# Kernel optimization log

Measured on AMD Instinct MI355X. Metric: run time of the kernel, lower is better.

The kernel has to match this reference:

```python
import jax, jax.numpy as jnp
import numpy as np

N, E, G = 100000, 1600000, 256   # nodes, edges, graphs
D, H, OUT, STEPS = 128, 128, 2, 4
EPS = 1e-5


def _bn(x, g, b):
    # BatchNorm1d training-mode math: biased batch stats
    mu = jnp.mean(x, axis=0)
    var = jnp.var(x, axis=0)
    return g * (x - mu) * jax.lax.rsqrt(var + EPS) + b


def setup_inputs() -> dict:
    key = jax.random.key(0)
    ks = jax.random.split(key, 20)
    s = 0.05
    return {
        "x": jax.random.normal(ks[0], (N, D), dtype=jnp.float32),
        "edge_index": jax.random.randint(ks[1], (2, E), 0, N, dtype=jnp.int32),
        "batch": jnp.sort(jax.random.randint(ks[2], (N,), 0, G, dtype=jnp.int32)),
        "W_in": jax.random.normal(ks[3], (H, D), dtype=jnp.float32) * s,
        "b_in": jnp.zeros((H,), jnp.float32),
        "bn1_g": jnp.ones((H,), jnp.float32),
        "bn1_b": jnp.zeros((H,), jnp.float32),
        "ggc_w": jax.random.normal(ks[4], (STEPS, H, H), dtype=jnp.float32) * s,
        "gru_wih": jax.random.normal(ks[5], (3 * H, H), dtype=jnp.float32) * s,
        "gru_whh": jax.random.normal(ks[6], (3 * H, H), dtype=jnp.float32) * s,
        "gru_bih": jnp.zeros((3 * H,), jnp.float32),
        "gru_bhh": jnp.zeros((3 * H,), jnp.float32),
        "bn2_g": jnp.ones((H,), jnp.float32),
        "bn2_b": jnp.zeros((H,), jnp.float32),
        "W1": jax.random.normal(ks[7], (H, 2 * H), dtype=jnp.float32) * s,
        "b1": jnp.zeros((H,), jnp.float32),
        "bn3_g": jnp.ones((H,), jnp.float32),
        "bn3_b": jnp.zeros((H,), jnp.float32),
        "W2": jax.random.normal(ks[8], (OUT, H), dtype=jnp.float32) * s,
        "b2": jnp.zeros((OUT,), jnp.float32),
    }


def reference(x, edge_index, batch, W_in, b_in, bn1_g, bn1_b, ggc_w,
              gru_wih, gru_whh, gru_bih, gru_bhh, bn2_g, bn2_b,
              W1, b1, bn3_g, bn3_b, W2, b2):
    src, dst = edge_index[0], edge_index[1]

    h = x @ W_in.T + b_in
    h = jax.nn.relu(_bn(h, bn1_g, bn1_b))
    skip = h

    # GatedGraphConv: per-step linear -> scatter-add aggregation -> GRUCell
    for i in range(STEPS):
        m = h @ ggc_w[i]                                   # [N,H]
        agg = jax.ops.segment_sum(m[src], dst, num_segments=N)  # [N,H]
        gi = agg @ gru_wih.T + gru_bih                     # [N,3H]
        gh = h @ gru_whh.T + gru_bhh                       # [N,3H]
        i_r, i_z, i_n = jnp.split(gi, 3, axis=1)
        h_r, h_z, h_n = jnp.split(gh, 3, axis=1)
        r = jax.nn.sigmoid(i_r + h_r)
        z = jax.nn.sigmoid(i_z + h_z)
        n = jnp.tanh(i_n + r * h_n)
        h = (1.0 - z) * n + z * h

    h = jax.nn.relu(_bn(h, bn2_g, bn2_b) + skip)

    # global_mean_pool (source uses it for both "mean" and "max" branches)
    cnt = jnp.maximum(jax.ops.segment_sum(jnp.ones((N,), h.dtype), batch, num_segments=G), 1.0)
    mean = jax.ops.segment_sum(h, batch, num_segments=G) / cnt[:, None]  # [G,H]
    pooled = jnp.concatenate([mean, mean], axis=1)                        # [G,2H]

    y = jax.nn.relu(_bn(pooled @ W1.T + b1, bn3_g, bn3_b))
    return y @ W2.T + b2
```

## Files before the change

kernel.cpp:

```cpp
#include <hip/hip_runtime.h>
#include <math.h>


#define EPSV 1e-5f

typedef __attribute__((ext_vector_type(8))) short bf16x8;
typedef __attribute__((ext_vector_type(4))) float f32x4;

__device__ __forceinline__ float fsig(float x){
  return 1.0f/(1.0f+__expf(-x));
}
__device__ __forceinline__ float ftanh(float x){
  float ax = fabsf(x);
  float e = __expf(-2.0f*ax);
  float r = (1.0f-e)/(1.0f+e);
  return copysignf(r, x);
}
__device__ __forceinline__ unsigned short bf16rne(float x){
  unsigned u = __float_as_uint(x);
  unsigned r = (u + 0x7FFFu + ((u>>16)&1u)) >> 16;
  return (unsigned short)r;
}
__device__ __forceinline__ float bf16tof(unsigned short h){
  return __uint_as_float(((unsigned)h)<<16);
}

__global__ void k_zero(float* __restrict__ p, int n){
  int i = blockIdx.x*256+threadIdx.x;
  if (i<n) p[i]=0.0f;
}

__global__ void k_prep(const float* __restrict__ Win, float* __restrict__ Wq,
                       const float* __restrict__ W1, float* __restrict__ W1cT){
  int i = blockIdx.x*256+threadIdx.x;
  if (i < 16384){
    int k=i>>7, j=i&127;
    Wq[(k>>2)*512 + j*4 + (k&3)] = Win[j*128+k];
  } else if (i < 32768){
    int r=i-16384; int j=r>>7, o=r&127;
    W1cT[j*128+o] = W1[o*256+j] + W1[o*256+128+j];
  }
}

__global__ void k_prepB(const float* __restrict__ ggc, const float* __restrict__ wih,
                        const float* __restrict__ whh,
                        short* __restrict__ Bhi, short* __restrict__ Blo){
  int i = blockIdx.x*256+threadIdx.x;
  int st = i>>17;
  int r  = i&131071;
  int k  = r>>9;
  int c  = r&511;
  int gr = c>>7, j = c&127;
  float val = 0.f;
  if (k<128){
    if (gr<3){
      const float* g = ggc + st*16384 + k*128;
      const float* w = wih + (gr*128+j)*128;
      float acc=0.f;
      for (int m=0;m<128;m++) acc += g[m]*w[m];
      val = acc;
    }
  } else {
    int kh = k-128;
    if (gr!=2){
      int gate = (gr==3)?2:gr;
      val = whh[(gate*128+j)*128 + kh];
    }
  }
  unsigned short h = bf16rne(val);
  unsigned short lo = bf16rne(val - bf16tof(h));
  size_t off = (size_t)st*131072 + ((size_t)(k>>5)*512 + (size_t)c)*32 + (size_t)(k&31);
  Bhi[off]=(short)h; Blo[off]=(short)lo;
}

__global__ __launch_bounds__(256,2) void k_gemm_in(
    const float* __restrict__ x, const float* __restrict__ Wq, const float* __restrict__ bin,
    float* __restrict__ X, float* __restrict__ sumP, float* __restrict__ sqP, int N)
{
  __shared__ __align__(16) float xl[32][128];
  __shared__ float red[2][128];
  int t=threadIdx.x;
  int nbase = blockIdx.x*32;
  for (int it=0; it<4; ++it){
    int f4 = it*256+t;
    int n = f4>>5; int k=(f4&31)*4;
    int gn=nbase+n;
    float4 v = make_float4(0.f,0.f,0.f,0.f);
    if (gn<N) v = *(const float4*)&x[(size_t)gn*128+k];
    *(float4*)&xl[n][k]=v;
  }
  __syncthreads();
  int j=t&127, half=t>>7, nb=half*16;
  float acc[16];
  #pragma unroll
  for (int q=0;q<16;q++) acc[q]=0.f;
  for (int k=0;k<128;k+=4){
    float4 w = *(const float4*)&Wq[(k>>2)*512 + j*4];
    #pragma unroll
    for (int q=0;q<16;q++){
      float4 xv = *(const float4*)&xl[nb+q][k];
      acc[q] += xv.x*w.x + xv.y*w.y + xv.z*w.z + xv.w*w.w;
    }
  }
  float bv = bin[j];
  float ts=0.f, tq=0.f;
  #pragma unroll
  for (int q=0;q<16;q++){
    int n=nbase+nb+q;
    if (n<N){
      float tv=acc[q]+bv;
      X[(size_t)n*128+j]=tv;
      ts+=tv; tq+=tv*tv;
    }
  }
  int p = (blockIdx.x&63)*128+j;
  red[half][j]=ts; __syncthreads();
  if (half==0) atomicAdd(&sumP[p], red[0][j]+red[1][j]);
  __syncthreads();
  red[half][j]=tq; __syncthreads();
  if (half==0) atomicAdd(&sqP[p], red[0][j]+red[1][j]);
}

__global__ void k_bn_fin(const float* __restrict__ sumP, const float* __restrict__ sqP, int P, float invcnt,
                         const float* __restrict__ g, const float* __restrict__ b,
                         float* __restrict__ sc, float* __restrict__ sh){
  int j = threadIdx.x;
  if (j>=128) return;
  float s=0.f,q=0.f;
  for (int p=0;p<P;p++){ s+=sumP[p*128+j]; q+=sqP[p*128+j]; }
  float mu = s*invcnt;
  float var = fmaxf(q*invcnt - mu*mu, 0.f);
  float scale = g[j]*rsqrtf(var+EPSV);
  sc[j]=scale; sh[j]=b[j]-mu*scale;
}

__global__ void k_apply_bn1(const float4* __restrict__ X, const float* __restrict__ sc,
                            const float* __restrict__ sh, float4* __restrict__ h0, int total4){
  int i = blockIdx.x*256+threadIdx.x;
  if (i>=total4) return;
  float4 t = X[i];
  int j0 = (i*4)&127;
  float4 s = *(const float4*)&sc[j0];
  float4 b = *(const float4*)&sh[j0];
  float4 o;
  o.x = fmaxf(t.x*s.x+b.x, 0.f);
  o.y = fmaxf(t.y*s.y+b.y, 0.f);
  o.z = fmaxf(t.z*s.z+b.z, 0.f);
  o.w = fmaxf(t.w*s.w+b.w, 0.f);
  h0[i]=o;
}

__global__ void k_hist(const int* __restrict__ dst, int* __restrict__ deg, int E){
  int e = blockIdx.x*256+threadIdx.x;
  if (e<E) atomicAdd(&deg[dst[e]], 1);
}
__global__ void k_scan1(const int* __restrict__ deg, int* __restrict__ rowptr, int* __restrict__ bsum, int N){
  __shared__ int tmp[256];
  int t=threadIdx.x; int n=blockIdx.x*256+t;
  int v = (n<N)?deg[n]:0;
  tmp[t]=v;
  __syncthreads();
  for (int o=1;o<256;o<<=1){
    int add = (t>=o)? tmp[t-o] : 0;
    __syncthreads();
    tmp[t]+=add;
    __syncthreads();
  }
  if (n<N) rowptr[n+1]=tmp[t];
  if (t==255) bsum[blockIdx.x]=tmp[255];
}
__global__ void k_scan2(int* bsum, int nb, int* rowptr){
  __shared__ int tmp[512];
  int t=threadIdx.x;
  int v = (t<nb)? bsum[t] : 0;
  tmp[t]=v; __syncthreads();
  for (int o=1;o<512;o<<=1){
    int add = (t>=o)? tmp[t-o] : 0;
    __syncthreads();
    tmp[t]+=add;
    __syncthreads();
  }
  if (t<nb) bsum[t]=tmp[t]-v;
  if (t==0) rowptr[0]=0;
}
__global__ void k_scan3(int* rowptr, const int* __restrict__ bsum, int N){
  int n = blockIdx.x*256+threadIdx.x;
  if (n<N) rowptr[n+1] += bsum[blockIdx.x];
}
__global__ void k_fill(const int* __restrict__ ei, int* __restrict__ deg,
                       const int* __restrict__ rowptr, int* __restrict__ col, int E){
  int e = blockIdx.x*256+threadIdx.x;
  if (e<E){
    int d = ei[E+e];
    int old = atomicSub(&deg[d],1);
    col[rowptr[d] + old - 1] = ei[e];
  }
}

__global__ __launch_bounds__(256,8) void k_agg(
    const float* __restrict__ h, float* __restrict__ s,
    const int* __restrict__ rowptr, const int* __restrict__ col, int N)
{
  int wave = (blockIdx.x*256+threadIdx.x)>>6;
  int lane = threadIdx.x&63;
  if (wave>=N) return;
  int e = rowptr[wave], e1 = rowptr[wave+1];
  float2 a0=make_float2(0.f,0.f), a1=a0, a2=a0, a3=a0;
  for (; e+3<e1; e+=4){
    int c0=col[e],c1=col[e+1],c2=col[e+2],c3=col[e+3];
    float2 v0 = *(const float2*)&h[(size_t)c0*128+lane*2];
    float2 v1 = *(const float2*)&h[(size_t)c1*128+lane*2];
    float2 v2 = *(const float2*)&h[(size_t)c2*128+lane*2];
    float2 v3 = *(const float2*)&h[(size_t)c3*128+lane*2];
    a0.x+=v0.x; a0.y+=v0.y; a1.x+=v1.x; a1.y+=v1.y;
    a2.x+=v2.x; a2.y+=v2.y; a3.x+=v3.x; a3.y+=v3.y;
  }
  for (; e<e1; e++){
    int c0=col[e];
    float2 v0 = *(const float2*)&h[(size_t)c0*128+lane*2];
    a0.x+=v0.x; a0.y+=v0.y;
  }
  float2 r;
  r.x=(a0.x+a1.x)+(a2.x+a3.x);
  r.y=(a0.y+a1.y)+(a2.y+a3.y);
  *(float2*)&s[(size_t)wave*128+lane*2]=r;
}

__global__ __launch_bounds__(256,2) void k_gru_mfma(
    const float* __restrict__ s, const float* __restrict__ hin, float* __restrict__ hout,
    const short* __restrict__ Bhi, const short* __restrict__ Blo,
    const float* __restrict__ bih, const float* __restrict__ bhh, int N,
    float* __restrict__ sumP, float* __restrict__ sqP)
{
  __shared__ short Ahi[32*256];
  __shared__ short Alo[32*256];
  int t = threadIdx.x;
  int nbase = blockIdx.x*32;

  for (int it=0; it<8; ++it){
    int f4 = it*256 + t;
    int row = f4>>6;
    int c4  = f4&63;
    int k   = c4*4;
    int n   = nbase + row;
    float4 v = make_float4(0.f,0.f,0.f,0.f);
    if (n < N){
      const float* src = (k<128) ? &s[(size_t)n*128 + k] : &hin[(size_t)n*128 + (k-128)];
      v = *(const float4*)src;
    }
    unsigned short h0=bf16rne(v.x), h1=bf16rne(v.y), h2=bf16rne(v.z), h3=bf16rne(v.w);
    unsigned short l0=bf16rne(v.x-bf16tof(h0)), l1=bf16rne(v.y-bf16tof(h1));
    unsigned short l2=bf16rne(v.z-bf16tof(h2)), l3=bf16rne(v.w-bf16tof(h3));
    int g = c4>>1, half = c4&1;
    int gs = g ^ (row&7);
    int off = row*256 + gs*8 + half*4;
    uint2 H; H.x = (unsigned)h0 | ((unsigned)h1<<16); H.y = (unsigned)h2 | ((unsigned)h3<<16);
    uint2 L; L.x = (unsigned)l0 | ((unsigned)l1<<16); L.y = (unsigned)l2 | ((unsigned)l3<<16);
    *(uint2*)&Ahi[off] = H;
    *(uint2*)&Alo[off] = L;
  }
  __syncthreads();

  int wv = t>>6, l = t&63;
  int lj = l&15, lk = l>>4;

  f32x4 acc[2][8];
  #pragma unroll
  for (int mt=0; mt<2; ++mt)
    #pragma unroll
    for (int nt=0; nt<8; ++nt)
      acc[mt][nt] = (f32x4){0.f,0.f,0.f,0.f};

  for (int kc=0; kc<8; ++kc){
    bf16x8 a_hi[2], a_lo[2];
    #pragma unroll
    for (int mt=0; mt<2; ++mt){
      int r = mt*16 + lj;
      int g = kc*4 + lk;
      int off = r*256 + ((g ^ (r&7))<<3);
      a_hi[mt] = *(bf16x8*)&Ahi[off];
      a_lo[mt] = *(bf16x8*)&Alo[off];
    }
    #pragma unroll
    for (int gr=0; gr<4; ++gr){
      #pragma unroll
      for (int jt=0; jt<2; ++jt){
        int nt = gr*2 + jt;
        int c  = gr*128 + wv*32 + jt*16 + lj;
        size_t boff = ((size_t)kc*512 + (size_t)c)*32 + (size_t)lk*8;
        bf16x8 b_hi = *(const bf16x8*)&Bhi[boff];
        bf16x8 b_lo = *(const bf16x8*)&Blo[boff];
        acc[0][nt] = __builtin_amdgcn_mfma_f32_16x16x32_bf16(a_hi[0], b_hi, acc[0][nt], 0,0,0);
        acc[1][nt] = __builtin_amdgcn_mfma_f32_16x16x32_bf16(a_hi[1], b_hi, acc[1][nt], 0,0,0);
        acc[0][nt] = __builtin_amdgcn_mfma_f32_16x16x32_bf16(a_lo[0], b_hi, acc[0][nt], 0,0,0);
        acc[1][nt] = __builtin_amdgcn_mfma_f32_16x16x32_bf16(a_lo[1], b_hi, acc[1][nt], 0,0,0);
        acc[0][nt] = __builtin_amdgcn_mfma_f32_16x16x32_bf16(a_hi[0], b_lo, acc[0][nt], 0,0,0);
        acc[1][nt] = __builtin_amdgcn_mfma_f32_16x16x32_bf16(a_hi[1], b_lo, acc[1][nt], 0,0,0);
      }
    }
  }

  #pragma unroll
  for (int jt=0; jt<2; ++jt){
    int j = wv*32 + jt*16 + lj;
    float br=bih[j], bz=bih[128+j], bn_=bih[256+j];
    float cr=bhh[j], cz=bhh[128+j], cn=bhh[256+j];
    float ts=0.f, tq=0.f;
    #pragma unroll
    for (int mt=0; mt<2; ++mt){
      #pragma unroll
      for (int rg=0; rg<4; ++rg){
        int n = nbase + mt*16 + lk*4 + rg;
        if (n < N){
          float r  = fsig(acc[mt][0+jt][rg] + br + cr);
          float z  = fsig(acc[mt][2+jt][rg] + bz + cz);
          float nn = ftanh(acc[mt][4+jt][rg] + bn_ + r*(acc[mt][6+jt][rg] + cn));
          float hold = hin[(size_t)n*128 + j];
          float hv = (1.f-z)*nn + z*hold;
          hout[(size_t)n*128 + j] = hv;
          ts += hv; tq += hv*hv;
        }
      }
    }
    if (sumP){
      atomicAdd(&sumP[(blockIdx.x&63)*128 + j], ts);
      atomicAdd(&sqP [(blockIdx.x&63)*128 + j], tq);
    }
  }
}

__global__ void k_bn2_pool(const float* __restrict__ hfin, const float* __restrict__ h0,
                           const int* __restrict__ batch, const float* __restrict__ sc,
                           const float* __restrict__ sh, float* __restrict__ pool,
                           float* __restrict__ cntf, int N){
  int t=threadIdx.x, j=t&127, half=t>>7;
  int n0 = blockIdx.x*256 + half*128;
  float scv=sc[j], shv=sh[j];
  int curg=-1; float acc=0.f, cacc=0.f;
  for (int r=0;r<128;r++){
    int n=n0+r; if (n>=N) break;
    int g = batch[n];
    float v = fmaxf(hfin[(size_t)n*128+j]*scv+shv + h0[(size_t)n*128+j], 0.f);
    if (g!=curg){
      if (curg>=0){
        atomicAdd(&pool[curg*128+j], acc);
        if (j==0) atomicAdd(&cntf[curg], cacc);
      }
      curg=g; acc=0.f; cacc=0.f;
    }
    acc+=v; cacc+=1.f;
  }
  if (curg>=0){
    atomicAdd(&pool[curg*128+j], acc);
    if (j==0) atomicAdd(&cntf[curg], cacc);
  }
}

__global__ void k_head1(const float* __restrict__ pool, const float* __restrict__ cntf,
                        const float* __restrict__ W1cT, const float* __restrict__ b1,
                        float* __restrict__ t3, float* __restrict__ sum3, float* __restrict__ sq3){
  __shared__ float mean[128];
  int g=blockIdx.x, o=threadIdx.x;
  float inv = 1.0f/fmaxf(cntf[g],1.0f);
  mean[o] = pool[g*128+o]*inv;
  __syncthreads();
  float acc=0.f;
  for (int jj=0;jj<128;jj++) acc += mean[jj]*W1cT[jj*128+o];
  float v = acc + b1[o];
  t3[g*128+o]=v;
  atomicAdd(&sum3[o], v);
  atomicAdd(&sq3[o], v*v);
}

__global__ void k_head2(const float* __restrict__ t3, const float* __restrict__ sc,
                        const float* __restrict__ sh, const float* __restrict__ W2,
                        const float* __restrict__ b2, float* __restrict__ out){
  __shared__ float y[128];
  int g=blockIdx.x, o=threadIdx.x;
  float v = fmaxf(t3[g*128+o]*sc[o]+sh[o], 0.f);
  y[o]=v; __syncthreads();
  if (o<2){
    float acc=b2[o];
    for (int k=0;k<128;k++) acc += y[k]*W2[o*128+k];
    out[g*2+o]=acc;
  }
}

extern "C" void kernel_launch(void* const* d_in, const int* in_sizes, int n_in,
                              void* d_out, int out_size, void* d_ws, size_t ws_size,
                              hipStream_t stream){
  (void)n_in; (void)ws_size;
  const float* x    = (const float*)d_in[0];
  const int*   ei   = (const int*)d_in[1];
  const int*   batch= (const int*)d_in[2];
  const float* W_in = (const float*)d_in[3];
  const float* b_in = (const float*)d_in[4];
  const float* bn1_g= (const float*)d_in[5];
  const float* bn1_b= (const float*)d_in[6];
  const float* ggc  = (const float*)d_in[7];
  const float* wih  = (const float*)d_in[8];
  const float* whh  = (const float*)d_in[9];
  const float* bih  = (const float*)d_in[10];
  const float* bhh  = (const float*)d_in[11];
  const float* bn2_g= (const float*)d_in[12];
  const float* bn2_b= (const float*)d_in[13];
  const float* W1   = (const float*)d_in[14];
  const float* b1   = (const float*)d_in[15];
  const float* bn3_g= (const float*)d_in[16];
  const float* bn3_b= (const float*)d_in[17];
  const float* W2   = (const float*)d_in[18];
  const float* b2   = (const float*)d_in[19];
  float* out = (float*)d_out;

  int N = in_sizes[0]/128;
  int E = in_sizes[1]/2;
  int G = out_size/2;

  char* ws = (char*)d_ws;
  size_t off=0;
  auto alloc=[&](size_t bytes)->char*{
    char* p = ws+off; off = (off+bytes+255) & ~(size_t)255; return p;
  };
  float* buf0 = (float*)alloc((size_t)N*128*4);
  float* h0   = (float*)alloc((size_t)N*128*4);
  float* buf2 = (float*)alloc((size_t)N*128*4);
  short* Bhi  = (short*)alloc((size_t)4*131072*2);
  short* Blo  = (short*)alloc((size_t)4*131072*2);
  float* Wq   = (float*)alloc((size_t)16384*4);
  float* W1cT = (float*)alloc((size_t)16384*4);
  int* rowptr = (int*)alloc((size_t)(N+1)*4);
  int* col    = (int*)alloc((size_t)E*4);
  int* bsum   = (int*)alloc((size_t)512*4);
  float* t3   = (float*)alloc((size_t)G*128*4);
  float* sc1 = (float*)alloc(512); float* sh1 = (float*)alloc(512);
  float* sc2 = (float*)alloc(512); float* sh2 = (float*)alloc(512);
  float* sc3 = (float*)alloc(512); float* sh3 = (float*)alloc(512);
  char* zstart = ws+off;
  int*   deg  = (int*)alloc((size_t)N*4);
  float* sumP1= (float*)alloc((size_t)64*128*4);
  float* sqP1 = (float*)alloc((size_t)64*128*4);
  float* sumP2= (float*)alloc((size_t)64*128*4);
  float* sqP2 = (float*)alloc((size_t)64*128*4);
  float* sum3 = (float*)alloc(512);
  float* sq3  = (float*)alloc(512);
  float* pool = (float*)alloc((size_t)G*128*4);
  float* cntf = (float*)alloc((size_t)G*4);
  char* zend = ws+off;
  int zwords = (int)((zend - zstart)/4);

  int nbScan  = (N+255)/256;
  int gridN32 = (N+31)/32;
  int gridAgg = (N*64+255)/256;

  k_zero<<<(zwords+255)/256,256,0,stream>>>((float*)zstart, zwords);
  k_prep<<<128,256,0,stream>>>(W_in, Wq, W1, W1cT);
  k_prepB<<<2048,256,0,stream>>>(ggc, wih, whh, Bhi, Blo);

  k_hist<<<(E+255)/256,256,0,stream>>>(ei+E, deg, E);
  k_scan1<<<nbScan,256,0,stream>>>(deg, rowptr, bsum, N);
  k_scan2<<<1,512,0,stream>>>(bsum, nbScan, rowptr);
  k_scan3<<<nbScan,256,0,stream>>>(rowptr, bsum, N);
  k_fill<<<(E+255)/256,256,0,stream>>>(ei, deg, rowptr, col, E);

  k_gemm_in<<<gridN32,256,0,stream>>>(x, Wq, b_in, buf0, sumP1, sqP1, N);
  k_bn_fin<<<1,128,0,stream>>>(sumP1, sqP1, 64, 1.0f/(float)N, bn1_g, bn1_b, sc1, sh1);
  k_apply_bn1<<<(N*128/4+255)/256,256,0,stream>>>((const float4*)buf0, sc1, sh1, (float4*)h0, N*128/4);

  k_agg<<<gridAgg,256,0,stream>>>(h0,   buf0, rowptr, col, N);
  k_gru_mfma<<<gridN32,256,0,stream>>>(buf0, h0,   buf0, Bhi+0*131072, Blo+0*131072, bih, bhh, N, nullptr, nullptr);
  k_agg<<<gridAgg,256,0,stream>>>(buf0, buf2, rowptr, col, N);
  k_gru_mfma<<<gridN32,256,0,stream>>>(buf2, buf0, buf2, Bhi+1*131072, Blo+1*131072, bih, bhh, N, nullptr, nullptr);
  k_agg<<<gridAgg,256,0,stream>>>(buf2, buf0, rowptr, col, N);
  k_gru_mfma<<<gridN32,256,0,stream>>>(buf0, buf2, buf0, Bhi+2*131072, Blo+2*131072, bih, bhh, N, nullptr, nullptr);
  k_agg<<<gridAgg,256,0,stream>>>(buf0, buf2, rowptr, col, N);
  k_gru_mfma<<<gridN32,256,0,stream>>>(buf2, buf0, buf2, Bhi+3*131072, Blo+3*131072, bih, bhh, N, sumP2, sqP2);

  k_bn_fin<<<1,128,0,stream>>>(sumP2, sqP2, 64, 1.0f/(float)N, bn2_g, bn2_b, sc2, sh2);
  k_bn2_pool<<<(N+255)/256,256,0,stream>>>(buf2, h0, batch, sc2, sh2, pool, cntf, N);
  k_head1<<<G,128,0,stream>>>(pool, cntf, W1cT, b1, t3, sum3, sq3);
  k_bn_fin<<<1,128,0,stream>>>(sum3, sq3, 1, 1.0f/(float)G, bn3_g, bn3_b, sc3, sh3);
  k_head2<<<G,128,0,stream>>>(t3, sc3, sh3, W2, b2, out);
}
```

Baseline: 1.494 ms.

## Skip zero weight blocks in GRU MFMA and stage h reuse and stores via LDS

```diff
diff --git a/kernel.cpp b/kernel.cpp
--- a/kernel.cpp
+++ b/kernel.cpp
@@ -232,8 +232,9 @@
     const float* __restrict__ bih, const float* __restrict__ bhh, int N,
     float* __restrict__ sumP, float* __restrict__ sqP)
 {
-  __shared__ short Ahi[32*256];
-  __shared__ short Alo[32*256];
+  __shared__ __align__(16) short Abuf[2*32*256];
+  short* Ahi = Abuf;
+  short* Alo = Abuf + 32*256;
   int t = threadIdx.x;
   int nbase = blockIdx.x*32;
 
@@ -271,7 +272,22 @@
     for (int nt=0; nt<8; ++nt)
       acc[mt][nt] = (f32x4){0.f,0.f,0.f,0.f};
 
-  for (int kc=0; kc<8; ++kc){
+#define DO_GR(GR_) { \
+    _Pragma("unroll") \
+    for (int jt=0; jt<2; ++jt){ \
+      int c  = (GR_)*128 + wv*32 + jt*16 + lj; \
+      size_t boff = ((size_t)kc*512 + (size_t)c)*32 + (size_t)lk*8; \
+      bf16x8 b_hi = *(const bf16x8*)&Bhi[boff]; \
+      bf16x8 b_lo = *(const bf16x8*)&Blo[boff]; \
+      acc[0][(GR_)*2+jt] = __builtin_amdgcn_mfma_f32_16x16x32_bf16(a_hi[0], b_hi, acc[0][(GR_)*2+jt], 0,0,0); \
+      acc[1][(GR_)*2+jt] = __builtin_amdgcn_mfma_f32_16x16x32_bf16(a_hi[1], b_hi, acc[1][(GR_)*2+jt], 0,0,0); \
+      acc[0][(GR_)*2+jt] = __builtin_amdgcn_mfma_f32_16x16x32_bf16(a_lo[0], b_hi, acc[0][(GR_)*2+jt], 0,0,0); \
+      acc[1][(GR_)*2+jt] = __builtin_amdgcn_mfma_f32_16x16x32_bf16(a_lo[1], b_hi, acc[1][(GR_)*2+jt], 0,0,0); \
+      acc[0][(GR_)*2+jt] = __builtin_amdgcn_mfma_f32_16x16x32_bf16(a_hi[0], b_lo, acc[0][(GR_)*2+jt], 0,0,0); \
+      acc[1][(GR_)*2+jt] = __builtin_amdgcn_mfma_f32_16x16x32_bf16(a_hi[1], b_lo, acc[1][(GR_)*2+jt], 0,0,0); \
+    } }
+
+  for (int kc=0; kc<4; ++kc){
     bf16x8 a_hi[2], a_lo[2];
     #pragma unroll
     for (int mt=0; mt<2; ++mt){
@@ -281,25 +297,40 @@
       a_hi[mt] = *(bf16x8*)&Ahi[off];
       a_lo[mt] = *(bf16x8*)&Alo[off];
     }
-    #pragma unroll
-    for (int gr=0; gr<4; ++gr){
+    DO_GR(0) DO_GR(1) DO_GR(2)
+  }
+  for (int kc=4; kc<8; ++kc){
+    bf16x8 a_hi[2], a_lo[2];
+    #pragma unroll
+    for (int mt=0; mt<2; ++mt){
+      int r = mt*16 + lj;
+      int g = kc*4 + lk;
+      int off = r*256 + ((g ^ (r&7))<<3);
+      a_hi[mt] = *(bf16x8*)&Ahi[off];
+      a_lo[mt] = *(bf16x8*)&Alo[off];
+    }
+    DO_GR(0) DO_GR(1) DO_GR(3)
+  }
+#undef DO_GR
+
+  float holdv[2][2][4];
+  #pragma unroll
+  for (int jt=0; jt<2; ++jt){
+    int j = wv*32 + jt*16 + lj;
+    int g = 16 + (j>>3);
+    int pos = j&7;
+    #pragma unroll
+    for (int mt=0; mt<2; ++mt){
       #pragma unroll
-      for (int jt=0; jt<2; ++jt){
-        int nt = gr*2 + jt;
-        int c  = gr*128 + wv*32 + jt*16 + lj;
-        size_t boff = ((size_t)kc*512 + (size_t)c)*32 + (size_t)lk*8;
-        bf16x8 b_hi = *(const bf16x8*)&Bhi[boff];
-        bf16x8 b_lo = *(const bf16x8*)&Blo[boff];
-        acc[0][nt] = __builtin_amdgcn_mfma_f32_16x16x32_bf16(a_hi[0], b_hi, acc[0][nt], 0,0,0);
-        acc[1][nt] = __builtin_amdgcn_mfma_f32_16x16x32_bf16(a_hi[1], b_hi, acc[1][nt], 0,0,0);
-        acc[0][nt] = __builtin_amdgcn_mfma_f32_16x16x32_bf16(a_lo[0], b_hi, acc[0][nt], 0,0,0);
-        acc[1][nt] = __builtin_amdgcn_mfma_f32_16x16x32_bf16(a_lo[1], b_hi, acc[1][nt], 0,0,0);
-        acc[0][nt] = __builtin_amdgcn_mfma_f32_16x16x32_bf16(a_hi[0], b_lo, acc[0][nt], 0,0,0);
-        acc[1][nt] = __builtin_amdgcn_mfma_f32_16x16x32_bf16(a_hi[1], b_lo, acc[1][nt], 0,0,0);
+      for (int rg=0; rg<4; ++rg){
+        int row = mt*16 + lk*4 + rg;
+        int off = row*256 + ((g ^ (row&7))<<3) + pos;
+        holdv[jt][mt][rg] = bf16tof((unsigned short)Ahi[off]) + bf16tof((unsigned short)Alo[off]);
       }
     }
   }
 
+  float hvv[2][2][4];
   #pragma unroll
   for (int jt=0; jt<2; ++jt){
     int j = wv*32 + jt*16 + lj;
@@ -310,21 +341,41 @@
     for (int mt=0; mt<2; ++mt){
       #pragma unroll
       for (int rg=0; rg<4; ++rg){
-        int n = nbase + mt*16 + lk*4 + rg;
-        if (n < N){
-          float r  = fsig(acc[mt][0+jt][rg] + br + cr);
-          float z  = fsig(acc[mt][2+jt][rg] + bz + cz);
-          float nn = ftanh(acc[mt][4+jt][rg] + bn_ + r*(acc[mt][6+jt][rg] + cn));
-          float hold = hin[(size_t)n*128 + j];
-          float hv = (1.f-z)*nn + z*hold;
-          hout[(size_t)n*128 + j] = hv;
-          ts += hv; tq += hv*hv;
-        }
+        float r  = fsig(acc[mt][0+jt][rg] + br + cr);
+        float z  = fsig(acc[mt][2+jt][rg] + bz + cz);
+        float nn = ftanh(acc[mt][4+jt][rg] + bn_ + r*(acc[mt][6+jt][rg] + cn));
+        float hv = (1.f-z)*nn + z*holdv[jt][mt][rg];
+        hvv[jt][mt][rg] = hv;
+        ts += hv; tq += hv*hv;
       }
     }
     if (sumP){
       atomicAdd(&sumP[(blockIdx.x&63)*128 + j], ts);
       atomicAdd(&sqP [(blockIdx.x&63)*128 + j], tq);
+    }
+  }
+
+  __syncthreads();
+  float* O = (float*)Abuf;
+  #pragma unroll
+  for (int jt=0; jt<2; ++jt){
+    int j = wv*32 + jt*16 + lj;
+    #pragma unroll
+    for (int mt=0; mt<2; ++mt){
+      #pragma unroll
+      for (int rg=0; rg<4; ++rg){
+        int row = mt*16 + lk*4 + rg;
+        O[row*132 + j] = hvv[jt][mt][rg];
+      }
+    }
+  }
+  __syncthreads();
+  for (int it=0; it<4; ++it){
+    int idx = it*256 + t;
+    int row = idx>>5, c4 = idx&31;
+    int n = nbase + row;
+    if (n < N){
+      *(float4*)&hout[(size_t)n*128 + c4*4] = *(float4*)&O[row*132 + c4*4];
     }
   }
 }
```

After: 1.449 ms. 3.0% less time.
